# Performance work log

Hardware: AMD Instinct MI355X
Metric: run time of the kernel (lower is better)

Reference implementation:

```python
import jax, jax.numpy as jnp
import numpy as np

B, H, S, D = 2, 16, 2048, 64

def setup_inputs() -> dict:
    key = jax.random.key(0)
    kq, kk, kv = jax.random.split(key, 3)
    query = jax.random.normal(kq, (B, H, S, D), dtype=jnp.float32)
    k_ = jax.random.normal(kk, (B, H, S, D), dtype=jnp.float32)
    value = jax.random.normal(kv, (B, H, S, D), dtype=jnp.float32)
    # causal bool mask: True = masked (matches torch masked_fill semantics)
    attn_mask = jnp.triu(jnp.ones((S, S), dtype=bool), k=1)
    # no padding (all False) so no softmax row is fully masked
    key_padding_mask = jnp.zeros((B, S), dtype=bool)
    return {"query": query, "key": k_, "value": value,
            "attn_mask": attn_mask, "key_padding_mask": key_padding_mask}

def reference(query, key, value, attn_mask, key_padding_mask):
    scale = query.shape[-1] ** -0.5
    # [B,H,Sq,Sk] scores
    scores = jnp.einsum('bhqd,bhkd->bhqk', query, key) * scale
    scores = jnp.where(key_padding_mask[:, None, None, :], -jnp.inf, scores)
    scores = jnp.where(attn_mask, -jnp.inf, scores)
    attn = jax.nn.softmax(scores, axis=-1)
    # dropout=0.0 -> identity in eval/math
    return jnp.einsum('bhqk,bhkd->bhqd', attn, value)
```

## Files before the change

kernel.cpp:

```cpp
#include <hip/hip_runtime.h>
#include <hip/hip_bf16.h>


#define BHN 32
#define SEQ 2048
#define DIM 64
#define NW  4
#define LSTR 72

typedef __attribute__((ext_vector_type(8)))  short    short8;
typedef __attribute__((ext_vector_type(4)))  short    short4v;
typedef __attribute__((ext_vector_type(4)))  float    float4v;
typedef __attribute__((ext_vector_type(16))) float    f32x16;
typedef __attribute__((ext_vector_type(4)))  unsigned uint4v;

__device__ __forceinline__ short f2b(float x) {
  __hip_bfloat16 h = __float2bfloat16(x);
  return __builtin_bit_cast(short, h);
}

__global__ __launch_bounds__(256) void prep_kernel(
    const float* __restrict__ K, const float* __restrict__ V,
    __hip_bfloat16* __restrict__ Kb, __hip_bfloat16* __restrict__ Vt) {
  __shared__ float t[64][65];
  const int bh = blockIdx.x, j = blockIdx.y, tid = threadIdx.x;
  const int r = tid >> 2, seg = (tid & 3) * 16;
  const size_t base = (size_t)bh * SEQ * DIM;
  {
    const float* ks = K + base + (size_t)(j * 64 + r) * DIM + seg;
    float4v k0 = *(const float4v*)(ks + 0);
    float4v k1 = *(const float4v*)(ks + 4);
    float4v k2 = *(const float4v*)(ks + 8);
    float4v k3 = *(const float4v*)(ks + 12);
    short8 a, b;
    a[0]=f2b(k0[0]); a[1]=f2b(k0[1]); a[2]=f2b(k0[2]); a[3]=f2b(k0[3]);
    a[4]=f2b(k1[0]); a[5]=f2b(k1[1]); a[6]=f2b(k1[2]); a[7]=f2b(k1[3]);
    b[0]=f2b(k2[0]); b[1]=f2b(k2[1]); b[2]=f2b(k2[2]); b[3]=f2b(k2[3]);
    b[4]=f2b(k3[0]); b[5]=f2b(k3[1]); b[6]=f2b(k3[2]); b[7]=f2b(k3[3]);
    __hip_bfloat16* kd = Kb + base + (size_t)(j * 64 + r) * DIM + seg;
    *(short8*)kd = a;
    *(short8*)(kd + 8) = b;
  }
  {
    const float* src = V + base + (size_t)(j * 64 + r) * DIM + seg;
    float4v f0 = *(const float4v*)(src + 0);
    float4v f1 = *(const float4v*)(src + 4);
    float4v f2 = *(const float4v*)(src + 8);
    float4v f3 = *(const float4v*)(src + 12);
    *(float4v*)&t[r][seg + 0]  = f0;
    *(float4v*)&t[r][seg + 4]  = f1;
    *(float4v*)&t[r][seg + 8]  = f2;
    *(float4v*)&t[r][seg + 12] = f3;
    __syncthreads();
    short8 o0, o1;
    #pragma unroll
    for (int i = 0; i < 8; ++i) o0[i] = f2b(t[seg + i][r]);
    #pragma unroll
    for (int i = 0; i < 8; ++i) o1[i] = f2b(t[seg + 8 + i][r]);
    __hip_bfloat16* dst = Vt + (size_t)bh * DIM * SEQ + (size_t)r * SEQ + j * 64 + seg;
    *(short8*)dst = o0;
    *(short8*)(dst + 8) = o1;
  }
}

__global__ __launch_bounds__(256, 2) void fattn6(
    const float* __restrict__ Qg, const __hip_bfloat16* __restrict__ Kb,
    const __hip_bfloat16* __restrict__ Vt, float* __restrict__ Og) {
  __shared__ alignas(16) __hip_bfloat16 kt[2][64][LSTR];
  __shared__ alignas(16) __hip_bfloat16 vt[2][64][LSTR];
  __shared__ float lbuf[NW][32];

  const int bh   = blockIdx.x;
  const int qt   = gridDim.y - 1 - blockIdx.y;
  const int tid  = threadIdx.x;
  const int w    = tid >> 6;
  const int lane = tid & 63;
  const int l31  = lane & 31;
  const int hi   = lane >> 5;
  const size_t base  = (size_t)bh * SEQ * DIM;
  const size_t baseV = (size_t)bh * DIM * SEQ;
  const int q0   = qt * 128;
  const int jmax = 2 * qt + 1;

  const float QSCALE = 0.125f * 1.44269504088896340736f;

  short8 qf[4];
  {
    const float* qp = Qg + base + (size_t)(q0 + 32 * w + l31) * DIM + 8 * hi;
    #pragma unroll
    for (int s = 0; s < 4; ++s) {
      float4v f0 = *(const float4v*)(qp + 16 * s);
      float4v f1 = *(const float4v*)(qp + 16 * s + 4);
      short8 qv;
      qv[0] = f2b(f0[0] * QSCALE); qv[1] = f2b(f0[1] * QSCALE);
      qv[2] = f2b(f0[2] * QSCALE); qv[3] = f2b(f0[3] * QSCALE);
      qv[4] = f2b(f1[0] * QSCALE); qv[5] = f2b(f1[1] * QSCALE);
      qv[6] = f2b(f1[2] * QSCALE); qv[7] = f2b(f1[3] * QSCALE);
      qf[s] = qv;
    }
  }

  f32x16 o0, o1;
  #pragma unroll
  for (int i = 0; i < 16; ++i) { o0[i] = 0.f; o1[i] = 0.f; }
  float acc_l = 0.f;

  const int srow = tid >> 2;
  const int scol = (tid & 3) * 16;

  short8 ka0, ka1, va0, va1;
  {
    const __hip_bfloat16* kp = Kb + base + (size_t)srow * DIM + scol;
    ka0 = *(const short8*)kp; ka1 = *(const short8*)(kp + 8);
    const __hip_bfloat16* vp = Vt + baseV + (size_t)srow * SEQ + scol;
    va0 = *(const short8*)vp; va1 = *(const short8*)(vp + 8);
  }
  *(short8*)&kt[0][srow][scol]     = ka0;
  *(short8*)&kt[0][srow][scol + 8] = ka1;
  *(short8*)&vt[0][srow][scol]     = va0;
  *(short8*)&vt[0][srow][scol + 8] = va1;
  __syncthreads();

  for (int j = 0; j <= jmax; ++j) {
    const int cur = j & 1;

    if (j < jmax) {
      const int kb = (j + 1) * 64;
      const __hip_bfloat16* kp = Kb + base + (size_t)(kb + srow) * DIM + scol;
      ka0 = *(const short8*)kp; ka1 = *(const short8*)(kp + 8);
      const __hip_bfloat16* vp = Vt + baseV + (size_t)srow * SEQ + kb + scol;
      va0 = *(const short8*)vp; va1 = *(const short8*)(vp + 8);
    }

    const bool act = (64 * j <= q0 + 32 * w + 31);
    unsigned pw[16];

    if (act) {
      f32x16 p0, p1;
      #pragma unroll
      for (int i = 0; i < 16; ++i) { p0[i] = 0.f; p1[i] = 0.f; }
      __builtin_amdgcn_s_setprio(1);
      #pragma unroll
      for (int s = 0; s < 4; ++s) {
        short8 a0 = *(const short8*)&kt[cur][l31][16 * s + 8 * hi];
        short8 a1 = *(const short8*)&kt[cur][32 + l31][16 * s + 8 * hi];
        p0 = __builtin_amdgcn_mfma_f32_32x32x16_bf16(a0, qf[s], p0, 0, 0, 0);
        p1 = __builtin_amdgcn_mfma_f32_32x32x16_bf16(a1, qf[s], p1, 0, 0, 0);
      }
      __builtin_amdgcn_s_setprio(0);

      if (64 * j + 63 > q0 + 32 * w) {
        const int qg  = q0 + 32 * w + l31;
        const int kb0 = 64 * j + 4 * hi;
        #pragma unroll
        for (int r = 0; r < 16; ++r) {
          const int kr = kb0 + (r & 3) + 8 * (r >> 2);
          if (kr > qg)      p0[r] = -1e30f;
          if (kr + 32 > qg) p1[r] = -1e30f;
        }
      }

      #pragma unroll
      for (int i = 0; i < 16; ++i) {
        p0[i] = __builtin_amdgcn_exp2f(p0[i]);
        p1[i] = __builtin_amdgcn_exp2f(p1[i]);
      }
      #pragma unroll
      for (int i = 0; i < 8; ++i)
        asm("v_cvt_pk_bf16_f32 %0, %1, %2"
            : "=v"(pw[i]) : "v"(p0[2 * i]), "v"(p0[2 * i + 1]));
      #pragma unroll
      for (int i = 0; i < 8; ++i)
        asm("v_cvt_pk_bf16_f32 %0, %1, %2"
            : "=v"(pw[8 + i]) : "v"(p1[2 * i]), "v"(p1[2 * i + 1]));

      float rs = 0.f;
      #pragma unroll
      for (int i = 0; i < 16; ++i) {
        rs += __builtin_bit_cast(float, pw[i] << 16);
        rs += __builtin_bit_cast(float, pw[i] & 0xffff0000u);
      }
      rs += __shfl_xor(rs, 32, 64);
      acc_l += rs;
    }

    if (j < jmax) {
      const int nb = cur ^ 1;
      *(short8*)&kt[nb][srow][scol]     = ka0;
      *(short8*)&kt[nb][srow][scol + 8] = ka1;
      *(short8*)&vt[nb][srow][scol]     = va0;
      *(short8*)&vt[nb][srow][scol + 8] = va1;
    }

    if (act) {
      #pragma unroll
      for (int t = 0; t < 4; ++t) {
        const unsigned x0 = __shfl_xor(pw[4 * t + 0], 32, 64);
        const unsigned x1 = __shfl_xor(pw[4 * t + 1], 32, 64);
        const unsigned x2 = __shfl_xor(pw[4 * t + 2], 32, 64);
        const unsigned x3 = __shfl_xor(pw[4 * t + 3], 32, 64);
        const unsigned f0 = hi ? x2 : pw[4 * t + 0];
        const unsigned f1 = hi ? x3 : pw[4 * t + 1];
        const unsigned f2 = hi ? pw[4 * t + 2] : x0;
        const unsigned f3 = hi ? pw[4 * t + 3] : x1;
        uint4v u = {f0, f1, f2, f3};
        short8 pa = __builtin_bit_cast(short8, u);
        short8 b0 = *(const short8*)&vt[cur][l31][16 * t + 8 * hi];
        short8 b1 = *(const short8*)&vt[cur][32 + l31][16 * t + 8 * hi];
        __builtin_amdgcn_s_setprio(1);
        o0 = __builtin_amdgcn_mfma_f32_32x32x16_bf16(pa, b0, o0, 0, 0, 0);
        o1 = __builtin_amdgcn_mfma_f32_32x32x16_bf16(pa, b1, o1, 0, 0, 0);
        __builtin_amdgcn_s_setprio(0);
      }
    }
    __syncthreads();
  }

  if (lane < 32) lbuf[w][l31] = acc_l;
  __syncthreads();
  const float* lb = lbuf[w];
  float* op = Og + base + (size_t)(q0 + 32 * w) * DIM + l31;
  #pragma unroll
  for (int r = 0; r < 16; ++r) {
    const int row = (r & 3) + 8 * (r >> 2) + 4 * hi;
    const float iv = 1.0f / lb[row];
    op[(size_t)row * DIM]      = o0[r] * iv;
    op[(size_t)row * DIM + 32] = o1[r] * iv;
  }
}

__global__ __launch_bounds__(256) void fattn_ref(
    const float* __restrict__ Qg, const float* __restrict__ Kg,
    const float* __restrict__ Vg, float* __restrict__ Og) {
  __shared__ alignas(16) __hip_bfloat16 kt[64][LSTR];
  __shared__ alignas(16) __hip_bfloat16 vt[64][LSTR];
  __shared__ alignas(16) __hip_bfloat16 pt[NW][16][LSTR];

  const int bh   = blockIdx.x;
  const int qt   = gridDim.y - 1 - blockIdx.y;
  const int tid  = threadIdx.x;
  const int wave = tid >> 6;
  const int lane = tid & 63;
  const int ln   = lane & 15;
  const int quad = lane >> 4;
  const size_t base = (size_t)bh * SEQ * DIM;
  const int q0 = qt * 64;

  const float QSCALE = 0.125f * 1.44269504088896340736f;
  short8 qf[2];
  {
    const int qrow = q0 + wave * 16 + ln;
    const float* qp = Qg + base + (size_t)qrow * DIM + quad * 8;
    #pragma unroll
    for (int kk = 0; kk < 2; ++kk) {
      float4v f0 = *(const float4v*)(qp + kk * 32);
      float4v f1 = *(const float4v*)(qp + kk * 32 + 4);
      short8 qv;
      qv[0] = f2b(f0[0] * QSCALE); qv[1] = f2b(f0[1] * QSCALE);
      qv[2] = f2b(f0[2] * QSCALE); qv[3] = f2b(f0[3] * QSCALE);
      qv[4] = f2b(f1[0] * QSCALE); qv[5] = f2b(f1[1] * QSCALE);
      qv[6] = f2b(f1[2] * QSCALE); qv[7] = f2b(f1[3] * QSCALE);
      qf[kk] = qv;
    }
  }
  float4v o[4];
  #pragma unroll
  for (int dt = 0; dt < 4; ++dt) { float4v z = {0.f,0.f,0.f,0.f}; o[dt] = z; }
  float l_i[4] = {0.f, 0.f, 0.f, 0.f};

  for (int j = 0; j <= qt; ++j) {
    const int kbase = j * 64;
    __syncthreads();
    {
      const int r = tid >> 4, c = (tid & 15) * 4;
      #pragma unroll
      for (int it = 0; it < 4; ++it) {
        const int row = it * 16 + r;
        float4v f = *(const float4v*)(Kg + base + (size_t)(kbase + row) * DIM + c);
        short4v sv; sv[0]=f2b(f[0]); sv[1]=f2b(f[1]); sv[2]=f2b(f[2]); sv[3]=f2b(f[3]);
        *(short4v*)&kt[row][c] = sv;
      }
      const int d = tid & 63, s0 = (tid >> 6) * 4;
      #pragma unroll
      for (int it = 0; it < 4; ++it) {
        const int sk = it * 16 + s0;
        short4v sv;
        sv[0] = f2b(Vg[base + (size_t)(kbase + sk + 0) * DIM + d]);
        sv[1] = f2b(Vg[base + (size_t)(kbase + sk + 1) * DIM + d]);
        sv[2] = f2b(Vg[base + (size_t)(kbase + sk + 2) * DIM + d]);
        sv[3] = f2b(Vg[base + (size_t)(kbase + sk + 3) * DIM + d]);
        *(short4v*)&vt[d][sk] = sv;
      }
    }
    __syncthreads();

    float4v s[4];
    #pragma unroll
    for (int nt = 0; nt < 4; ++nt) {
      short8 b0 = *(const short8*)&kt[nt * 16 + ln][quad * 8];
      short8 b1 = *(const short8*)&kt[nt * 16 + ln][32 + quad * 8];
      float4v acc = {0.f,0.f,0.f,0.f};
      acc = __builtin_amdgcn_mfma_f32_16x16x32_bf16(qf[0], b0, acc, 0, 0, 0);
      acc = __builtin_amdgcn_mfma_f32_16x16x32_bf16(qf[1], b1, acc, 0, 0, 0);
      s[nt] = acc;
    }
    if (j == qt) {
      #pragma unroll
      for (int nt = 0; nt < 4; ++nt) {
        const int col = nt * 16 + ln;
        #pragma unroll
        for (int rg = 0; rg < 4; ++rg)
          if (col > wave * 16 + quad * 4 + rg) s[nt][rg] = -1e30f;
      }
    }
    #pragma unroll
    for (int rg = 0; rg < 4; ++rg) {
      float p0 = __builtin_amdgcn_exp2f(s[0][rg]);
      float p1 = __builtin_amdgcn_exp2f(s[1][rg]);
      float p2 = __builtin_amdgcn_exp2f(s[2][rg]);
      float p3 = __builtin_amdgcn_exp2f(s[3][rg]);
      s[0][rg]=p0; s[1][rg]=p1; s[2][rg]=p2; s[3][rg]=p3;
      float rs = (p0 + p1) + (p2 + p3);
      rs += __shfl_xor(rs, 1, 64); rs += __shfl_xor(rs, 2, 64);
      rs += __shfl_xor(rs, 4, 64); rs += __shfl_xor(rs, 8, 64);
      l_i[rg] += rs;
    }
    #pragma unroll
    for (int nt = 0; nt < 4; ++nt)
      #pragma unroll
      for (int rg = 0; rg < 4; ++rg)
        pt[wave][quad * 4 + rg][nt * 16 + ln] = __float2bfloat16(s[nt][rg]);
    short8 pa0 = *(const short8*)&pt[wave][ln][quad * 8];
    short8 pa1 = *(const short8*)&pt[wave][ln][32 + quad * 8];
    #pragma unroll
    for (int dt = 0; dt < 4; ++dt) {
      short8 vb0 = *(const short8*)&vt[dt * 16 + ln][quad * 8];
      short8 vb1 = *(const short8*)&vt[dt * 16 + ln][32 + quad * 8];
      o[dt] = __builtin_amdgcn_mfma_f32_16x16x32_bf16(pa0, vb0, o[dt], 0, 0, 0);
      o[dt] = __builtin_amdgcn_mfma_f32_16x16x32_bf16(pa1, vb1, o[dt], 0, 0, 0);
    }
  }
  #pragma unroll
  for (int rg = 0; rg < 4; ++rg) {
    const float inv = 1.0f / l_i[rg];
    const int row = q0 + wave * 16 + quad * 4 + rg;
    float* op = Og + base + (size_t)row * DIM + ln;
    #pragma unroll
    for (int dt = 0; dt < 4; ++dt) op[dt * 16] = o[dt][rg] * inv;
  }
}

extern "C" void kernel_launch(void* const* d_in, const int* in_sizes, int n_in,
                              void* d_out, int out_size, void* d_ws, size_t ws_size,
                              hipStream_t stream) {
  (void)in_sizes; (void)n_in; (void)out_size;
  const float* Q = (const float*)d_in[0];
  const float* K = (const float*)d_in[1];
  const float* V = (const float*)d_in[2];
  float* O = (float*)d_out;
  const size_t need = (size_t)2 * BHN * SEQ * DIM * sizeof(__hip_bfloat16);
  if (ws_size >= need) {
    __hip_bfloat16* Kb = (__hip_bfloat16*)d_ws;
    __hip_bfloat16* Vt = Kb + (size_t)BHN * SEQ * DIM;
    prep_kernel<<<dim3(BHN, SEQ / 64), 256, 0, stream>>>(K, V, Kb, Vt);
    fattn6<<<dim3(BHN, SEQ / 128), 256, 0, stream>>>(Q, Kb, Vt, O);
  } else {
    fattn_ref<<<dim3(BHN, SEQ / 64), 256, 0, stream>>>(Q, K, V, O);
  }
}
```

Measured before the change: 147.7 us.

## Use 64-row query tiles with two waves and compute row sums via MFMA

The attention kernel now processes 64 query rows per block with 128 threads (two waves) instead of 128 rows with four waves, doubling the grid and removing per-wave inactive-tile checks. The prep kernel permutes V columns so P fragments feed the PV MFMA directly, removing cross-lane shuffles. Row sums are accumulated with an extra MFMA against a ones vector instead of scalar adds and an LDS reduction. This adds a third MFMA per step and halves K/V tile reuse per block, in exchange for more blocks and less shuffle/VALU work.

```diff
diff --git a/kernel.cpp b/kernel.cpp
--- a/kernel.cpp
+++ b/kernel.cpp
@@ -5,7 +5,6 @@
 #define BHN 32
 #define SEQ 2048
 #define DIM 64
-#define NW  4
 #define LSTR 72
 
 typedef __attribute__((ext_vector_type(8)))  short    short8;
@@ -52,23 +51,25 @@
     *(float4v*)&t[r][seg + 8]  = f2;
     *(float4v*)&t[r][seg + 12] = f3;
     __syncthreads();
-    short8 o0, o1;
-    #pragma unroll
-    for (int i = 0; i < 8; ++i) o0[i] = f2b(t[seg + i][r]);
-    #pragma unroll
-    for (int i = 0; i < 8; ++i) o1[i] = f2b(t[seg + 8 + i][r]);
+    short8 n0, n1;
+    #pragma unroll
+    for (int i = 0; i < 4; ++i) {
+      n0[i]     = f2b(t[seg + i][r]);
+      n0[4 + i] = f2b(t[seg + 8 + i][r]);
+      n1[i]     = f2b(t[seg + 4 + i][r]);
+      n1[4 + i] = f2b(t[seg + 12 + i][r]);
+    }
     __hip_bfloat16* dst = Vt + (size_t)bh * DIM * SEQ + (size_t)r * SEQ + j * 64 + seg;
-    *(short8*)dst = o0;
-    *(short8*)(dst + 8) = o1;
-  }
-}
-
-__global__ __launch_bounds__(256, 2) void fattn6(
+    *(short8*)dst = n0;
+    *(short8*)(dst + 8) = n1;
+  }
+}
+
+__global__ __launch_bounds__(128, 2) void fattn7(
     const float* __restrict__ Qg, const __hip_bfloat16* __restrict__ Kb,
     const __hip_bfloat16* __restrict__ Vt, float* __restrict__ Og) {
   __shared__ alignas(16) __hip_bfloat16 kt[2][64][LSTR];
   __shared__ alignas(16) __hip_bfloat16 vt[2][64][LSTR];
-  __shared__ float lbuf[NW][32];
 
   const int bh   = blockIdx.x;
   const int qt   = gridDim.y - 1 - blockIdx.y;
@@ -79,8 +80,7 @@
   const int hi   = lane >> 5;
   const size_t base  = (size_t)bh * SEQ * DIM;
   const size_t baseV = (size_t)bh * DIM * SEQ;
-  const int q0   = qt * 128;
-  const int jmax = 2 * qt + 1;
+  const int q0   = qt * 64;
 
   const float QSCALE = 0.125f * 1.44269504088896340736f;
 
@@ -100,130 +100,114 @@
     }
   }
 
-  f32x16 o0, o1;
-  #pragma unroll
-  for (int i = 0; i < 16; ++i) { o0[i] = 0.f; o1[i] = 0.f; }
-  float acc_l = 0.f;
-
-  const int srow = tid >> 2;
-  const int scol = (tid & 3) * 16;
-
-  short8 ka0, ka1, va0, va1;
+  short8 ones;
+  #pragma unroll
+  for (int x = 0; x < 8; ++x) ones[x] = (short)0x3F80;
+
+  f32x16 o0, o1, l16;
+  #pragma unroll
+  for (int i = 0; i < 16; ++i) { o0[i] = 0.f; o1[i] = 0.f; l16[i] = 0.f; }
+
+  const int srow = tid >> 1;
+  const int scol = (tid & 1) * 32;
+
+  short8 sk[4], sv[4];
   {
     const __hip_bfloat16* kp = Kb + base + (size_t)srow * DIM + scol;
-    ka0 = *(const short8*)kp; ka1 = *(const short8*)(kp + 8);
     const __hip_bfloat16* vp = Vt + baseV + (size_t)srow * SEQ + scol;
-    va0 = *(const short8*)vp; va1 = *(const short8*)(vp + 8);
-  }
-  *(short8*)&kt[0][srow][scol]     = ka0;
-  *(short8*)&kt[0][srow][scol + 8] = ka1;
-  *(short8*)&vt[0][srow][scol]     = va0;
-  *(short8*)&vt[0][srow][scol + 8] = va1;
+    #pragma unroll
+    for (int i = 0; i < 4; ++i) { sk[i] = *(const short8*)(kp + 8 * i); }
+    #pragma unroll
+    for (int i = 0; i < 4; ++i) { sv[i] = *(const short8*)(vp + 8 * i); }
+  }
+  #pragma unroll
+  for (int i = 0; i < 4; ++i) {
+    *(short8*)&kt[0][srow][scol + 8 * i] = sk[i];
+    *(short8*)&vt[0][srow][scol + 8 * i] = sv[i];
+  }
   __syncthreads();
 
-  for (int j = 0; j <= jmax; ++j) {
+  for (int j = 0; j <= qt; ++j) {
     const int cur = j & 1;
 
-    if (j < jmax) {
+    if (j < qt) {
       const int kb = (j + 1) * 64;
       const __hip_bfloat16* kp = Kb + base + (size_t)(kb + srow) * DIM + scol;
-      ka0 = *(const short8*)kp; ka1 = *(const short8*)(kp + 8);
       const __hip_bfloat16* vp = Vt + baseV + (size_t)srow * SEQ + kb + scol;
-      va0 = *(const short8*)vp; va1 = *(const short8*)(vp + 8);
-    }
-
-    const bool act = (64 * j <= q0 + 32 * w + 31);
+      #pragma unroll
+      for (int i = 0; i < 4; ++i) { sk[i] = *(const short8*)(kp + 8 * i); }
+      #pragma unroll
+      for (int i = 0; i < 4; ++i) { sv[i] = *(const short8*)(vp + 8 * i); }
+    }
+
+    f32x16 p0, p1;
+    #pragma unroll
+    for (int i = 0; i < 16; ++i) { p0[i] = 0.f; p1[i] = 0.f; }
+    __builtin_amdgcn_s_setprio(1);
+    #pragma unroll
+    for (int s = 0; s < 4; ++s) {
+      short8 a0 = *(const short8*)&kt[cur][l31][16 * s + 8 * hi];
+      short8 a1 = *(const short8*)&kt[cur][32 + l31][16 * s + 8 * hi];
+      p0 = __builtin_amdgcn_mfma_f32_32x32x16_bf16(a0, qf[s], p0, 0, 0, 0);
+      p1 = __builtin_amdgcn_mfma_f32_32x32x16_bf16(a1, qf[s], p1, 0, 0, 0);
+    }
+    __builtin_amdgcn_s_setprio(0);
+
+    if (j == qt) {
+      const int qg  = q0 + 32 * w + l31;
+      const int kb0 = 64 * j + 4 * hi;
+      #pragma unroll
+      for (int r = 0; r < 16; ++r) {
+        const int kr = kb0 + (r & 3) + 8 * (r >> 2);
+        if (kr > qg)      p0[r] = -1e30f;
+        if (kr + 32 > qg) p1[r] = -1e30f;
+      }
+    }
+
+    #pragma unroll
+    for (int i = 0; i < 16; ++i) {
+      p0[i] = __builtin_amdgcn_exp2f(p0[i]);
+      p1[i] = __builtin_amdgcn_exp2f(p1[i]);
+    }
     unsigned pw[16];
-
-    if (act) {
-      f32x16 p0, p1;
-      #pragma unroll
-      for (int i = 0; i < 16; ++i) { p0[i] = 0.f; p1[i] = 0.f; }
-      __builtin_amdgcn_s_setprio(1);
-      #pragma unroll
-      for (int s = 0; s < 4; ++s) {
-        short8 a0 = *(const short8*)&kt[cur][l31][16 * s + 8 * hi];
-        short8 a1 = *(const short8*)&kt[cur][32 + l31][16 * s + 8 * hi];
-        p0 = __builtin_amdgcn_mfma_f32_32x32x16_bf16(a0, qf[s], p0, 0, 0, 0);
-        p1 = __builtin_amdgcn_mfma_f32_32x32x16_bf16(a1, qf[s], p1, 0, 0, 0);
-      }
-      __builtin_amdgcn_s_setprio(0);
-
-      if (64 * j + 63 > q0 + 32 * w) {
-        const int qg  = q0 + 32 * w + l31;
-        const int kb0 = 64 * j + 4 * hi;
-        #pragma unroll
-        for (int r = 0; r < 16; ++r) {
-          const int kr = kb0 + (r & 3) + 8 * (r >> 2);
-          if (kr > qg)      p0[r] = -1e30f;
-          if (kr + 32 > qg) p1[r] = -1e30f;
-        }
-      }
-
-      #pragma unroll
-      for (int i = 0; i < 16; ++i) {
-        p0[i] = __builtin_amdgcn_exp2f(p0[i]);
-        p1[i] = __builtin_amdgcn_exp2f(p1[i]);
-      }
-      #pragma unroll
-      for (int i = 0; i < 8; ++i)
-        asm("v_cvt_pk_bf16_f32 %0, %1, %2"
-            : "=v"(pw[i]) : "v"(p0[2 * i]), "v"(p0[2 * i + 1]));
-      #pragma unroll
-      for (int i = 0; i < 8; ++i)
-        asm("v_cvt_pk_bf16_f32 %0, %1, %2"
-            : "=v"(pw[8 + i]) : "v"(p1[2 * i]), "v"(p1[2 * i + 1]));
-
-      float rs = 0.f;
-      #pragma unroll
-      for (int i = 0; i < 16; ++i) {
-        rs += __builtin_bit_cast(float, pw[i] << 16);
-        rs += __builtin_bit_cast(float, pw[i] & 0xffff0000u);
-      }
-      rs += __shfl_xor(rs, 32, 64);
-      acc_l += rs;
-    }
-
-    if (j < jmax) {
+    #pragma unroll
+    for (int i = 0; i < 8; ++i)
+      asm("v_cvt_pk_bf16_f32 %0, %1, %2"
+          : "=v"(pw[i]) : "v"(p0[2 * i]), "v"(p0[2 * i + 1]));
+    #pragma unroll
+    for (int i = 0; i < 8; ++i)
+      asm("v_cvt_pk_bf16_f32 %0, %1, %2"
+          : "=v"(pw[8 + i]) : "v"(p1[2 * i]), "v"(p1[2 * i + 1]));
+
+    if (j < qt) {
       const int nb = cur ^ 1;
-      *(short8*)&kt[nb][srow][scol]     = ka0;
-      *(short8*)&kt[nb][srow][scol + 8] = ka1;
-      *(short8*)&vt[nb][srow][scol]     = va0;
-      *(short8*)&vt[nb][srow][scol + 8] = va1;
-    }
-
-    if (act) {
-      #pragma unroll
-      for (int t = 0; t < 4; ++t) {
-        const unsigned x0 = __shfl_xor(pw[4 * t + 0], 32, 64);
-        const unsigned x1 = __shfl_xor(pw[4 * t + 1], 32, 64);
-        const unsigned x2 = __shfl_xor(pw[4 * t + 2], 32, 64);
-        const unsigned x3 = __shfl_xor(pw[4 * t + 3], 32, 64);
-        const unsigned f0 = hi ? x2 : pw[4 * t + 0];
-        const unsigned f1 = hi ? x3 : pw[4 * t + 1];
-        const unsigned f2 = hi ? pw[4 * t + 2] : x0;
-        const unsigned f3 = hi ? pw[4 * t + 3] : x1;
-        uint4v u = {f0, f1, f2, f3};
-        short8 pa = __builtin_bit_cast(short8, u);
-        short8 b0 = *(const short8*)&vt[cur][l31][16 * t + 8 * hi];
-        short8 b1 = *(const short8*)&vt[cur][32 + l31][16 * t + 8 * hi];
-        __builtin_amdgcn_s_setprio(1);
-        o0 = __builtin_amdgcn_mfma_f32_32x32x16_bf16(pa, b0, o0, 0, 0, 0);
-        o1 = __builtin_amdgcn_mfma_f32_32x32x16_bf16(pa, b1, o1, 0, 0, 0);
-        __builtin_amdgcn_s_setprio(0);
-      }
-    }
+      #pragma unroll
+      for (int i = 0; i < 4; ++i) {
+        *(short8*)&kt[nb][srow][scol + 8 * i] = sk[i];
+        *(short8*)&vt[nb][srow][scol + 8 * i] = sv[i];
+      }
+    }
+
+    __builtin_amdgcn_s_setprio(1);
+    #pragma unroll
+    for (int t = 0; t < 4; ++t) {
+      uint4v u = {pw[4 * t], pw[4 * t + 1], pw[4 * t + 2], pw[4 * t + 3]};
+      short8 pa = __builtin_bit_cast(short8, u);
+      short8 b0 = *(const short8*)&vt[cur][l31][16 * t + 8 * hi];
+      short8 b1 = *(const short8*)&vt[cur][32 + l31][16 * t + 8 * hi];
+      o0  = __builtin_amdgcn_mfma_f32_32x32x16_bf16(pa, b0, o0, 0, 0, 0);
+      o1  = __builtin_amdgcn_mfma_f32_32x32x16_bf16(pa, b1, o1, 0, 0, 0);
+      l16 = __builtin_amdgcn_mfma_f32_32x32x16_bf16(pa, ones, l16, 0, 0, 0);
+    }
+    __builtin_amdgcn_s_setprio(0);
     __syncthreads();
   }
 
-  if (lane < 32) lbuf[w][l31] = acc_l;
-  __syncthreads();
-  const float* lb = lbuf[w];
   float* op = Og + base + (size_t)(q0 + 32 * w) * DIM + l31;
   #pragma unroll
   for (int r = 0; r < 16; ++r) {
     const int row = (r & 3) + 8 * (r >> 2) + 4 * hi;
-    const float iv = 1.0f / lb[row];
+    const float iv = 1.0f / l16[r];
     op[(size_t)row * DIM]      = o0[r] * iv;
     op[(size_t)row * DIM + 32] = o1[r] * iv;
   }
@@ -234,7 +218,7 @@
     const float* __restrict__ Vg, float* __restrict__ Og) {
   __shared__ alignas(16) __hip_bfloat16 kt[64][LSTR];
   __shared__ alignas(16) __hip_bfloat16 vt[64][LSTR];
-  __shared__ alignas(16) __hip_bfloat16 pt[NW][16][LSTR];
+  __shared__ alignas(16) __hip_bfloat16 pt[4][16][LSTR];
 
   const int bh   = blockIdx.x;
   const int qt   = gridDim.y - 1 - blockIdx.y;
@@ -363,7 +347,7 @@
     __hip_bfloat16* Kb = (__hip_bfloat16*)d_ws;
     __hip_bfloat16* Vt = Kb + (size_t)BHN * SEQ * DIM;
     prep_kernel<<<dim3(BHN, SEQ / 64), 256, 0, stream>>>(K, V, Kb, Vt);
-    fattn6<<<dim3(BHN, SEQ / 128), 256, 0, stream>>>(Q, Kb, Vt, O);
+    fattn7<<<dim3(BHN, SEQ / 64), 128, 0, stream>>>(Q, Kb, Vt, O);
   } else {
     fattn_ref<<<dim3(BHN, SEQ / 64), 256, 0, stream>>>(Q, K, V, O);
   }
```

Measured after the change: 140.1 us. -5.1%, faster.
